# Kernel optimization log

Hardware: AMD Instinct MI355X
Metric: run time of the kernel (lower is better)

The kernel has to match this reference:

```python
import jax, jax.numpy as jnp
import numpy as np
import math

D_MODEL = 1024
NUM_HEADS = 16
D_K = D_MODEL // NUM_HEADS
B, S = 2, 2048


def _linear_weight(key, out_f, in_f):
    return jax.random.normal(key, (out_f, in_f), jnp.float32) * math.sqrt(2.0 / in_f)


def setup_inputs() -> dict:
    key = jax.random.key(0)
    ks = jax.random.split(key, 5)
    x = jax.random.normal(ks[0], (B, S, D_MODEL), jnp.float32)
    return {
        "x": x,
        "Wq": _linear_weight(ks[1], D_MODEL, D_MODEL),
        "bq": jnp.zeros((D_MODEL,), jnp.float32),
        "Wk": _linear_weight(ks[2], D_MODEL, D_MODEL),
        "bk": jnp.zeros((D_MODEL,), jnp.float32),
        "Wv": _linear_weight(ks[3], D_MODEL, D_MODEL),
        "bv": jnp.zeros((D_MODEL,), jnp.float32),
        "Wo": _linear_weight(ks[4], D_MODEL, D_MODEL),
        "bo": jnp.zeros((D_MODEL,), jnp.float32),
    }


def reference(x, Wq, bq, Wk, bk, Wv, bv, Wo, bo):
    b, s, _ = x.shape
    # Projections: x @ W.T + b (CustomLinear stores weight as (out, in))
    q = jnp.einsum("bsd,ed->bse", x, Wq) + bq
    k = jnp.einsum("bsd,ed->bse", x, Wk) + bk
    v = jnp.einsum("bsd,ed->bse", x, Wv) + bv
    # (b, h, s, d_k)
    q = q.reshape(b, s, NUM_HEADS, D_K).transpose(0, 2, 1, 3)
    k = k.reshape(b, s, NUM_HEADS, D_K).transpose(0, 2, 1, 3)
    v = v.reshape(b, s, NUM_HEADS, D_K).transpose(0, 2, 1, 3)
    # Scaled dot-product attention with fully materialized scores (faithful)
    scores = jnp.einsum("bhqd,bhkd->bhqk", q, k) / math.sqrt(D_K)
    attn = jax.nn.softmax(scores, axis=-1)
    out = jnp.einsum("bhqk,bhkd->bhqd", attn, v)
    out = out.transpose(0, 2, 1, 3).reshape(b, s, D_MODEL)
    return jnp.einsum("bsd,ed->bse", out, Wo) + bo
```

## Files before the change

kernel.cpp:

```cpp
#include <hip/hip_runtime.h>
#include <hip/hip_bf16.h>

using bf16 = __hip_bfloat16;
typedef __attribute__((ext_vector_type(8))) short short8;
typedef __attribute__((ext_vector_type(4))) short s4v;
typedef __attribute__((ext_vector_type(4))) float float4v;
typedef __attribute__((ext_vector_type(4))) float f32x4;

#define MFMA16(a, b, c) __builtin_amdgcn_mfma_f32_16x16x32_bf16((a), (b), (c), 0, 0, 0)

#define GLD_LDS16(g, l)                                            \
    __builtin_amdgcn_global_load_lds(                              \
        (const __attribute__((address_space(1))) void*)(g),        \
        (__attribute__((address_space(3))) void*)(l), 16, 0, 0)

constexpr int Bc = 2;
constexpr int Sc = 2048;
constexpr int Hc = 16;
constexpr int DKc = 64;
constexpr int Dc = 1024;
constexpr size_t MEG = 1024 * 1024;

union BFU { bf16 h; short s; };

__device__ inline short bfbits(float f) {
    BFU u; u.h = __float2bfloat16(f); return u.s;
}

__device__ inline short8 load_cvt8(const float* __restrict__ p) {
    f32x4 a = *(const f32x4*)p;
    f32x4 b = *(const f32x4*)(p + 4);
    short8 r;
    r[0] = bfbits(a[0]); r[1] = bfbits(a[1]); r[2] = bfbits(a[2]); r[3] = bfbits(a[3]);
    r[4] = bfbits(b[0]); r[5] = bfbits(b[1]); r[6] = bfbits(b[2]); r[7] = bfbits(b[3]);
    return r;
}

__global__ __launch_bounds__(256) void cvt_kernel(
    const float* __restrict__ x, const float* __restrict__ Wq,
    const float* __restrict__ Wk, const float* __restrict__ Wv,
    const float* __restrict__ Wo, bf16* __restrict__ dst)
{
    const size_t i = ((size_t)blockIdx.x * 256 + threadIdx.x) * 8;
    const float* s;
    if      (i < 4 * MEG) s = x  + i;
    else if (i < 5 * MEG) s = Wq + (i - 4 * MEG);
    else if (i < 6 * MEG) s = Wk + (i - 5 * MEG);
    else if (i < 7 * MEG) s = Wv + (i - 6 * MEG);
    else                  s = Wo + (i - 7 * MEG);
    *(short8*)(dst + i) = load_cvt8(s);
}

__global__ __launch_bounds__(256) void qkv_gemm_kernel(
    const bf16* __restrict__ x,
    const bf16* __restrict__ Wq, const float* __restrict__ bq,
    const bf16* __restrict__ Wk, const float* __restrict__ bk,
    const bf16* __restrict__ Wv, const float* __restrict__ bv,
    bf16* __restrict__ q_ws, bf16* __restrict__ k_ws, bf16* __restrict__ v_ws)
{
    constexpr int BM = 128, BN = 128, BK = 32;
    __shared__ __align__(16) bf16 sA[BM * BK];
    __shared__ __align__(16) bf16 sB[BN * BK];

    const int bx = blockIdx.x;
    const int sel = bx >> 3;
    const int n0 = (bx & 7) * BN;
    const int m0 = blockIdx.y * BM;

    const bf16* __restrict__ Wsel = (sel == 0) ? Wq : ((sel == 1) ? Wk : Wv);
    const float* __restrict__ bsel = (sel == 0) ? bq : ((sel == 1) ? bk : bv);

    const int t = threadIdx.x;
    const int lane = t & 63;
    const int wave = t >> 6;
    const int ln = lane & 15;
    const int qd = lane >> 4;
    const int wm = (wave >> 1) * 64;
    const int wn = (wave & 1) * 64;

    const int gr = lane >> 2;
    const int gc = (lane & 3) * 8;

    float4v acc[4][4];
#pragma unroll
    for (int i = 0; i < 4; i++)
#pragma unroll
        for (int j = 0; j < 4; j++) acc[i][j] = (float4v)0.0f;

    for (int kk = 0; kk < Dc; kk += BK) {
        __syncthreads();
#pragma unroll
        for (int cc = 0; cc < 2; cc++) {
            const int c = wave * 2 + cc;
            GLD_LDS16(x    + (size_t)(m0 + c * 16 + gr) * Dc + kk + gc, &sA[c * 512]);
            GLD_LDS16(Wsel + (size_t)(n0 + c * 16 + gr) * Dc + kk + gc, &sB[c * 512]);
        }
        __syncthreads();

        short8 af[4], wf[4];
#pragma unroll
        for (int i = 0; i < 4; i++)
            af[i] = *(const short8*)&sA[(wm + i * 16 + ln) * BK + qd * 8];
#pragma unroll
        for (int j = 0; j < 4; j++)
            wf[j] = *(const short8*)&sB[(wn + j * 16 + ln) * BK + qd * 8];
#pragma unroll
        for (int i = 0; i < 4; i++)
#pragma unroll
            for (int j = 0; j < 4; j++)
                acc[i][j] = MFMA16(af[i], wf[j], acc[i][j]);
    }

    constexpr float QSCALE = 0.125f * 1.44269504088896f;

#pragma unroll
    for (int j = 0; j < 4; j++) {
        const int n = n0 + wn + j * 16 + ln;
        const float bias = bsel[n];
        const int h_ = n >> 6, d_ = n & 63;
#pragma unroll
        for (int i = 0; i < 4; i++) {
            const int mbase = m0 + wm + i * 16 + qd * 4;
#pragma unroll
            for (int r = 0; r < 4; r++) {
                const int m = mbase + r;
                const int b_ = m >> 11, s_ = m & 2047;
                float v = acc[i][j][r] + bias;
                if (sel == 0) v *= QSCALE;
                const bf16 o = __float2bfloat16(v);
                if (sel == 0)
                    q_ws[(((size_t)(b_ * Hc + h_)) * Sc + s_) * DKc + d_] = o;
                else if (sel == 1)
                    k_ws[(((size_t)(b_ * Hc + h_)) * Sc + s_) * DKc + d_] = o;
                else
                    v_ws[(((size_t)(b_ * Hc + h_)) * DKc + d_) * Sc + s_] = o;
            }
        }
    }
}

__global__ __launch_bounds__(256) void attn_kernel(
    const bf16* __restrict__ q_ws, const bf16* __restrict__ k_ws,
    const bf16* __restrict__ v_ws, bf16* __restrict__ ao_ws)
{
    constexpr int LQP = 76;
    __shared__ __align__(16) bf16 sQ[128 * 64];
    __shared__ __align__(16) bf16 sK[2][64 * 64];
    __shared__ __align__(16) bf16 sV[2][64 * 64];
    __shared__ __align__(16) short sP[4][32 * LQP];

    const int bh = blockIdx.x;
    const int qt = blockIdx.y;
    const int t = threadIdx.x;
    const int lane = t & 63;
    const int wave = t >> 6;
    const int ln = lane & 15;
    const int qd = lane >> 4;
    short* const sPw = sP[wave];

    const bf16* __restrict__ Qbase = q_ws + (size_t)bh * Sc * DKc + qt * 128 * DKc;
    const bf16* __restrict__ Kbase = k_ws + (size_t)bh * Sc * DKc;
    const bf16* __restrict__ Vbase = v_ws + (size_t)bh * DKc * Sc;

    const int rloc = lane >> 3;
    const int blk = lane & 7;

    {
#pragma unroll
        for (int cc = 0; cc < 4; cc++) {
            const int c = wave * 4 + cc;
            const int row = c * 8 + rloc;
            const int gb = blk ^ (row & 7);
            GLD_LDS16(Qbase + (size_t)row * DKc + gb * 8, &sQ[c * 512]);
        }
    }
    {
#pragma unroll
        for (int cc = 0; cc < 2; cc++) {
            const int c = wave * 2 + cc;
            const int row = c * 8 + rloc;
            const int gb = blk ^ (row & 7);
            GLD_LDS16(Kbase + (size_t)row * DKc + gb * 8, &sK[0][c * 512]);
            GLD_LDS16(Vbase + (size_t)row * Sc + gb * 8, &sV[0][c * 512]);
        }
    }

    short8 ones8;
    {
        const short ob = (ln == 0) ? (short)0x3F80 : (short)0;
#pragma unroll
        for (int i = 0; i < 8; i++) ones8[i] = ob;
    }

    float4v oacc[2][5];
#pragma unroll
    for (int mt = 0; mt < 2; mt++)
#pragma unroll
        for (int j = 0; j < 5; j++) oacc[mt][j] = (float4v)0.0f;

    for (int kt = 0; kt < Sc / 64; kt++) {
        const int cur = kt & 1;
        __syncthreads();
        if (kt + 1 < Sc / 64) {
            const int nxt = (kt + 1) & 1;
#pragma unroll
            for (int cc = 0; cc < 2; cc++) {
                const int c = wave * 2 + cc;
                const int row = c * 8 + rloc;
                const int gb = blk ^ (row & 7);
                GLD_LDS16(Kbase + (size_t)((kt + 1) * 64 + row) * DKc + gb * 8,
                          &sK[nxt][c * 512]);
                GLD_LDS16(Vbase + (size_t)row * Sc + (kt + 1) * 64 + gb * 8,
                          &sV[nxt][c * 512]);
            }
        }

        float4v sacc[2][4];
#pragma unroll
        for (int mt = 0; mt < 2; mt++)
#pragma unroll
            for (int j = 0; j < 4; j++) sacc[mt][j] = (float4v)0.0f;
#pragma unroll
        for (int ks = 0; ks < 2; ks++) {
            short8 bq[2];
#pragma unroll
            for (int mt = 0; mt < 2; mt++) {
                const int row = wave * 32 + mt * 16 + ln;
                bq[mt] = *(const short8*)
                    &sQ[row * 64 + (((ks * 4 + qd) ^ (row & 7)) << 3)];
            }
#pragma unroll
            for (int j = 0; j < 4; j++) {
                const int row = j * 16 + ln;
                const short8 ak = *(const short8*)
                    &sK[cur][row * 64 + (((ks * 4 + qd) ^ (row & 7)) << 3)];
                sacc[0][j] = MFMA16(ak, bq[0], sacc[0][j]);
                sacc[1][j] = MFMA16(ak, bq[1], sacc[1][j]);
            }
        }

#pragma unroll
        for (int mt = 0; mt < 2; mt++)
#pragma unroll
            for (int j = 0; j < 4; j++) {
                s4v pk;
#pragma unroll
                for (int r = 0; r < 4; r++)
                    pk[r] = bfbits(exp2f(sacc[mt][j][r]));
                *(s4v*)&sPw[(mt * 16 + ln) * LQP + j * 16 + qd * 4] = pk;
            }

#pragma unroll
        for (int ks = 0; ks < 2; ks++) {
            short8 ap[2];
#pragma unroll
            for (int mt = 0; mt < 2; mt++) {
                const s4v p0 = *(const s4v*)&sPw[(mt * 16 + ln) * LQP + ks * 32 + qd * 8];
                const s4v p1 = *(const s4v*)&sPw[(mt * 16 + ln) * LQP + ks * 32 + qd * 8 + 4];
                ap[mt][0] = p0[0]; ap[mt][1] = p0[1]; ap[mt][2] = p0[2]; ap[mt][3] = p0[3];
                ap[mt][4] = p1[0]; ap[mt][5] = p1[1]; ap[mt][6] = p1[2]; ap[mt][7] = p1[3];
            }
#pragma unroll
            for (int j = 0; j < 4; j++) {
                const int row = j * 16 + ln;
                const short8 bv_ = *(const short8*)
                    &sV[cur][row * 64 + (((ks * 4 + qd) ^ (row & 7)) << 3)];
                oacc[0][j] = MFMA16(ap[0], bv_, oacc[0][j]);
                oacc[1][j] = MFMA16(ap[1], bv_, oacc[1][j]);
            }
            oacc[0][4] = MFMA16(ap[0], ones8, oacc[0][4]);
            oacc[1][4] = MFMA16(ap[1], ones8, oacc[1][4]);
        }
    }

    const int b_ = bh >> 4, h_ = bh & 15;
#pragma unroll
    for (int mt = 0; mt < 2; mt++) {
#pragma unroll
        for (int r = 0; r < 4; r++) {
            const float l = __shfl(oacc[mt][4][r], lane & 48, 64);
            const float inv = 1.0f / l;
            const int s_ = qt * 128 + wave * 32 + mt * 16 + qd * 4 + r;
#pragma unroll
            for (int j = 0; j < 4; j++) {
                const int d_ = j * 16 + ln;
                ao_ws[(((size_t)(b_ * Sc + s_)) * Hc + h_) * DKc + d_] =
                    __float2bfloat16(oacc[mt][j][r] * inv);
            }
        }
    }
}

__global__ __launch_bounds__(256) void out_gemm_kernel(
    const bf16* __restrict__ A, const bf16* __restrict__ Wo,
    const float* __restrict__ bo, float* __restrict__ out)
{
    constexpr int BM = 128, BN = 128, BK = 32;
    __shared__ __align__(16) bf16 sA[BM * BK];
    __shared__ __align__(16) bf16 sB[BN * BK];

    const int n0 = blockIdx.x * BN;
    const int m0 = blockIdx.y * BM;

    const int t = threadIdx.x;
    const int lane = t & 63;
    const int wave = t >> 6;
    const int ln = lane & 15;
    const int qd = lane >> 4;
    const int wm = (wave >> 1) * 64;
    const int wn = (wave & 1) * 64;

    const int gr = lane >> 2;
    const int gc = (lane & 3) * 8;

    float4v acc[4][4];
#pragma unroll
    for (int i = 0; i < 4; i++)
#pragma unroll
        for (int j = 0; j < 4; j++) acc[i][j] = (float4v)0.0f;

    for (int kk = 0; kk < Dc; kk += BK) {
        __syncthreads();
#pragma unroll
        for (int cc = 0; cc < 2; cc++) {
            const int c = wave * 2 + cc;
            GLD_LDS16(A  + (size_t)(m0 + c * 16 + gr) * Dc + kk + gc, &sA[c * 512]);
            GLD_LDS16(Wo + (size_t)(n0 + c * 16 + gr) * Dc + kk + gc, &sB[c * 512]);
        }
        __syncthreads();

        short8 af[4], wf[4];
#pragma unroll
        for (int i = 0; i < 4; i++)
            af[i] = *(const short8*)&sA[(wm + i * 16 + ln) * BK + qd * 8];
#pragma unroll
        for (int j = 0; j < 4; j++)
            wf[j] = *(const short8*)&sB[(wn + j * 16 + ln) * BK + qd * 8];
#pragma unroll
        for (int i = 0; i < 4; i++)
#pragma unroll
            for (int j = 0; j < 4; j++)
                acc[i][j] = MFMA16(af[i], wf[j], acc[i][j]);
    }

#pragma unroll
    for (int j = 0; j < 4; j++) {
        const int n = n0 + wn + j * 16 + ln;
        const float bias = bo[n];
#pragma unroll
        for (int i = 0; i < 4; i++) {
            const int mbase = m0 + wm + i * 16 + qd * 4;
#pragma unroll
            for (int r = 0; r < 4; r++) {
                const int m = mbase + r;
                out[(size_t)m * Dc + n] = acc[i][j][r] + bias;
            }
        }
    }
}

extern "C" void kernel_launch(void* const* d_in, const int* in_sizes, int n_in,
                              void* d_out, int out_size, void* d_ws, size_t ws_size,
                              hipStream_t stream)
{
    const float* x  = (const float*)d_in[0];
    const float* Wq = (const float*)d_in[1];
    const float* bq = (const float*)d_in[2];
    const float* Wk = (const float*)d_in[3];
    const float* bk = (const float*)d_in[4];
    const float* Wv = (const float*)d_in[5];
    const float* bv = (const float*)d_in[6];
    const float* Wo = (const float*)d_in[7];
    const float* bo = (const float*)d_in[8];
    float* out = (float*)d_out;

    bf16* base  = (bf16*)d_ws;
    bf16* q_ws  = base;
    bf16* k_ws  = base + 4 * MEG;
    bf16* v_ws  = base + 8 * MEG;
    bf16* ao_ws = base + 12 * MEG;
    bf16* xb    = base + 16 * MEG;
    bf16* wqb   = base + 20 * MEG;
    bf16* wkb   = base + 21 * MEG;
    bf16* wvb   = base + 22 * MEG;
    bf16* wob   = base + 23 * MEG;

    cvt_kernel<<<dim3(4096), 256, 0, stream>>>(x, Wq, Wk, Wv, Wo, xb);
    qkv_gemm_kernel<<<dim3(24, 32), 256, 0, stream>>>(
        xb, wqb, bq, wkb, bk, wvb, bv, q_ws, k_ws, v_ws);
    attn_kernel<<<dim3(32, 16), 256, 0, stream>>>(q_ws, k_ws, v_ws, ao_ws);
    out_gemm_kernel<<<dim3(8, 32), 256, 0, stream>>>(ao_ws, wob, bo, out);
}
```

Baseline: 214.9 us.

## Split attention work across eight waves and vectorize transposed V stores

The attention kernel now launches 512 threads per block, so each of eight waves handles 16 query rows instead of each of four waves handling 32. This halves per-wave accumulator registers and adds latency hiding within a block. The cost is that each wave reuses each K/V LDS fragment across fewer MFMAs, and the block-wide barrier now covers more waves. Separately, the V projection epilogue packs four consecutive sequence elements into one 8-byte store instead of four scalar strided stores.

```diff
diff --git a/kernel.cpp b/kernel.cpp
--- a/kernel.cpp
+++ b/kernel.cpp
@@ -121,25 +121,32 @@
 #pragma unroll
         for (int i = 0; i < 4; i++) {
             const int mbase = m0 + wm + i * 16 + qd * 4;
-#pragma unroll
-            for (int r = 0; r < 4; r++) {
-                const int m = mbase + r;
-                const int b_ = m >> 11, s_ = m & 2047;
-                float v = acc[i][j][r] + bias;
-                if (sel == 0) v *= QSCALE;
-                const bf16 o = __float2bfloat16(v);
-                if (sel == 0)
-                    q_ws[(((size_t)(b_ * Hc + h_)) * Sc + s_) * DKc + d_] = o;
-                else if (sel == 1)
-                    k_ws[(((size_t)(b_ * Hc + h_)) * Sc + s_) * DKc + d_] = o;
-                else
-                    v_ws[(((size_t)(b_ * Hc + h_)) * DKc + d_) * Sc + s_] = o;
+            if (sel == 2) {
+                const int b_ = mbase >> 11, s_ = mbase & 2047;
+                s4v pk;
+#pragma unroll
+                for (int r = 0; r < 4; r++)
+                    pk[r] = bfbits(acc[i][j][r] + bias);
+                *(s4v*)&v_ws[(((size_t)(b_ * Hc + h_)) * DKc + d_) * Sc + s_] = pk;
+            } else {
+#pragma unroll
+                for (int r = 0; r < 4; r++) {
+                    const int m = mbase + r;
+                    const int b_ = m >> 11, s_ = m & 2047;
+                    float v = acc[i][j][r] + bias;
+                    if (sel == 0) v *= QSCALE;
+                    const bf16 o = __float2bfloat16(v);
+                    if (sel == 0)
+                        q_ws[(((size_t)(b_ * Hc + h_)) * Sc + s_) * DKc + d_] = o;
+                    else
+                        k_ws[(((size_t)(b_ * Hc + h_)) * Sc + s_) * DKc + d_] = o;
+                }
             }
         }
     }
 }
 
-__global__ __launch_bounds__(256) void attn_kernel(
+__global__ __launch_bounds__(512) void attn_kernel(
     const bf16* __restrict__ q_ws, const bf16* __restrict__ k_ws,
     const bf16* __restrict__ v_ws, bf16* __restrict__ ao_ws)
 {
@@ -147,7 +154,7 @@
     __shared__ __align__(16) bf16 sQ[128 * 64];
     __shared__ __align__(16) bf16 sK[2][64 * 64];
     __shared__ __align__(16) bf16 sV[2][64 * 64];
-    __shared__ __align__(16) short sP[4][32 * LQP];
+    __shared__ __align__(16) short sP[8][16 * LQP];
 
     const int bh = blockIdx.x;
     const int qt = blockIdx.y;
@@ -167,22 +174,18 @@
 
     {
 #pragma unroll
-        for (int cc = 0; cc < 4; cc++) {
-            const int c = wave * 4 + cc;
-            const int row = c * 8 + rloc;
-            const int gb = blk ^ (row & 7);
-            GLD_LDS16(Qbase + (size_t)row * DKc + gb * 8, &sQ[c * 512]);
-        }
-    }
-    {
-#pragma unroll
         for (int cc = 0; cc < 2; cc++) {
             const int c = wave * 2 + cc;
             const int row = c * 8 + rloc;
             const int gb = blk ^ (row & 7);
-            GLD_LDS16(Kbase + (size_t)row * DKc + gb * 8, &sK[0][c * 512]);
-            GLD_LDS16(Vbase + (size_t)row * Sc + gb * 8, &sV[0][c * 512]);
-        }
+            GLD_LDS16(Qbase + (size_t)row * DKc + gb * 8, &sQ[c * 512]);
+        }
+    }
+    {
+        const int row = wave * 8 + rloc;
+        const int gb = blk ^ (row & 7);
+        GLD_LDS16(Kbase + (size_t)row * DKc + gb * 8, &sK[0][wave * 512]);
+        GLD_LDS16(Vbase + (size_t)row * Sc + gb * 8, &sV[0][wave * 512]);
     }
 
     short8 ones8;
@@ -192,101 +195,78 @@
         for (int i = 0; i < 8; i++) ones8[i] = ob;
     }
 
-    float4v oacc[2][5];
-#pragma unroll
-    for (int mt = 0; mt < 2; mt++)
-#pragma unroll
-        for (int j = 0; j < 5; j++) oacc[mt][j] = (float4v)0.0f;
+    float4v oacc[5];
+#pragma unroll
+    for (int j = 0; j < 5; j++) oacc[j] = (float4v)0.0f;
 
     for (int kt = 0; kt < Sc / 64; kt++) {
         const int cur = kt & 1;
         __syncthreads();
         if (kt + 1 < Sc / 64) {
             const int nxt = (kt + 1) & 1;
-#pragma unroll
-            for (int cc = 0; cc < 2; cc++) {
-                const int c = wave * 2 + cc;
-                const int row = c * 8 + rloc;
-                const int gb = blk ^ (row & 7);
-                GLD_LDS16(Kbase + (size_t)((kt + 1) * 64 + row) * DKc + gb * 8,
-                          &sK[nxt][c * 512]);
-                GLD_LDS16(Vbase + (size_t)row * Sc + (kt + 1) * 64 + gb * 8,
-                          &sV[nxt][c * 512]);
-            }
-        }
-
-        float4v sacc[2][4];
-#pragma unroll
-        for (int mt = 0; mt < 2; mt++)
-#pragma unroll
-            for (int j = 0; j < 4; j++) sacc[mt][j] = (float4v)0.0f;
+            const int row = wave * 8 + rloc;
+            const int gb = blk ^ (row & 7);
+            GLD_LDS16(Kbase + (size_t)((kt + 1) * 64 + row) * DKc + gb * 8,
+                      &sK[nxt][wave * 512]);
+            GLD_LDS16(Vbase + (size_t)row * Sc + (kt + 1) * 64 + gb * 8,
+                      &sV[nxt][wave * 512]);
+        }
+
+        float4v sacc[4];
+#pragma unroll
+        for (int j = 0; j < 4; j++) sacc[j] = (float4v)0.0f;
 #pragma unroll
         for (int ks = 0; ks < 2; ks++) {
-            short8 bq[2];
-#pragma unroll
-            for (int mt = 0; mt < 2; mt++) {
-                const int row = wave * 32 + mt * 16 + ln;
-                bq[mt] = *(const short8*)
-                    &sQ[row * 64 + (((ks * 4 + qd) ^ (row & 7)) << 3)];
-            }
+            const int qrow = wave * 16 + ln;
+            const short8 bq = *(const short8*)
+                &sQ[qrow * 64 + (((ks * 4 + qd) ^ (qrow & 7)) << 3)];
 #pragma unroll
             for (int j = 0; j < 4; j++) {
                 const int row = j * 16 + ln;
                 const short8 ak = *(const short8*)
                     &sK[cur][row * 64 + (((ks * 4 + qd) ^ (row & 7)) << 3)];
-                sacc[0][j] = MFMA16(ak, bq[0], sacc[0][j]);
-                sacc[1][j] = MFMA16(ak, bq[1], sacc[1][j]);
+                sacc[j] = MFMA16(ak, bq, sacc[j]);
             }
         }
 
 #pragma unroll
-        for (int mt = 0; mt < 2; mt++)
-#pragma unroll
-            for (int j = 0; j < 4; j++) {
-                s4v pk;
-#pragma unroll
-                for (int r = 0; r < 4; r++)
-                    pk[r] = bfbits(exp2f(sacc[mt][j][r]));
-                *(s4v*)&sPw[(mt * 16 + ln) * LQP + j * 16 + qd * 4] = pk;
-            }
+        for (int j = 0; j < 4; j++) {
+            s4v pk;
+#pragma unroll
+            for (int r = 0; r < 4; r++)
+                pk[r] = bfbits(exp2f(sacc[j][r]));
+            *(s4v*)&sPw[ln * LQP + j * 16 + qd * 4] = pk;
+        }
 
 #pragma unroll
         for (int ks = 0; ks < 2; ks++) {
-            short8 ap[2];
-#pragma unroll
-            for (int mt = 0; mt < 2; mt++) {
-                const s4v p0 = *(const s4v*)&sPw[(mt * 16 + ln) * LQP + ks * 32 + qd * 8];
-                const s4v p1 = *(const s4v*)&sPw[(mt * 16 + ln) * LQP + ks * 32 + qd * 8 + 4];
-                ap[mt][0] = p0[0]; ap[mt][1] = p0[1]; ap[mt][2] = p0[2]; ap[mt][3] = p0[3];
-                ap[mt][4] = p1[0]; ap[mt][5] = p1[1]; ap[mt][6] = p1[2]; ap[mt][7] = p1[3];
-            }
+            const s4v p0 = *(const s4v*)&sPw[ln * LQP + ks * 32 + qd * 8];
+            const s4v p1 = *(const s4v*)&sPw[ln * LQP + ks * 32 + qd * 8 + 4];
+            short8 ap;
+            ap[0] = p0[0]; ap[1] = p0[1]; ap[2] = p0[2]; ap[3] = p0[3];
+            ap[4] = p1[0]; ap[5] = p1[1]; ap[6] = p1[2]; ap[7] = p1[3];
 #pragma unroll
             for (int j = 0; j < 4; j++) {
                 const int row = j * 16 + ln;
                 const short8 bv_ = *(const short8*)
                     &sV[cur][row * 64 + (((ks * 4 + qd) ^ (row & 7)) << 3)];
-                oacc[0][j] = MFMA16(ap[0], bv_, oacc[0][j]);
-                oacc[1][j] = MFMA16(ap[1], bv_, oacc[1][j]);
+                oacc[j] = MFMA16(ap, bv_, oacc[j]);
             }
-            oacc[0][4] = MFMA16(ap[0], ones8, oacc[0][4]);
-            oacc[1][4] = MFMA16(ap[1], ones8, oacc[1][4]);
+            oacc[4] = MFMA16(ap, ones8, oacc[4]);
         }
     }
 
     const int b_ = bh >> 4, h_ = bh & 15;
 #pragma unroll
-    for (int mt = 0; mt < 2; mt++) {
-#pragma unroll
-        for (int r = 0; r < 4; r++) {
-            const float l = __shfl(oacc[mt][4][r], lane & 48, 64);
-            const float inv = 1.0f / l;
-            const int s_ = qt * 128 + wave * 32 + mt * 16 + qd * 4 + r;
-#pragma unroll
-            for (int j = 0; j < 4; j++) {
-                const int d_ = j * 16 + ln;
-                ao_ws[(((size_t)(b_ * Sc + s_)) * Hc + h_) * DKc + d_] =
-                    __float2bfloat16(oacc[mt][j][r] * inv);
-            }
+    for (int r = 0; r < 4; r++) {
+        const float l = __shfl(oacc[4][r], lane & 48, 64);
+        const float inv = 1.0f / l;
+        const int s_ = qt * 128 + wave * 16 + qd * 4 + r;
+#pragma unroll
+        for (int j = 0; j < 4; j++) {
+            const int d_ = j * 16 + ln;
+            ao_ws[(((size_t)(b_ * Sc + s_)) * Hc + h_) * DKc + d_] =
+                __float2bfloat16(oacc[j][r] * inv);
         }
     }
 }
@@ -388,6 +368,6 @@
     cvt_kernel<<<dim3(4096), 256, 0, stream>>>(x, Wq, Wk, Wv, Wo, xb);
     qkv_gemm_kernel<<<dim3(24, 32), 256, 0, stream>>>(
         xb, wqb, bq, wkb, bk, wvb, bv, q_ws, k_ws, v_ws);
-    attn_kernel<<<dim3(32, 16), 256, 0, stream>>>(q_ws, k_ws, v_ws, ao_ws);
+    attn_kernel<<<dim3(32, 16), 512, 0, stream>>>(q_ws, k_ws, v_ws, ao_ws);
     out_gemm_kernel<<<dim3(8, 32), 256, 0, stream>>>(ao_ws, wob, bo, out);
 }
```

After: 200.4 us. 6.7% less time.
